# Kernel optimization log

Hardware: AMD Instinct MI355X
Metric: run time of the kernel (lower is better)

Reference implementation:

```python
import jax, jax.numpy as jnp
import numpy as np

T, B, D, H = 2048, 64, 256, 512

def setup_inputs() -> dict:
    key = jax.random.key(0)
    ks = jax.random.split(key, 4)
    s = 1.0 / np.sqrt(D + H)  # nn.Linear default uniform scale approximated with normal*s
    return {
        "x": jax.random.normal(ks[0], (T, B, D), dtype=jnp.float32),
        "h0": jnp.zeros((B, H), dtype=jnp.float32),
        "Wz": jax.random.normal(ks[1], (D + H, H), dtype=jnp.float32) * s,
        "bz": jnp.zeros((H,), dtype=jnp.float32),
        "Wr": jax.random.normal(ks[2], (D + H, H), dtype=jnp.float32) * s,
        "br": jnp.zeros((H,), dtype=jnp.float32),
        "Wh": jax.random.normal(ks[3], (D + H, H), dtype=jnp.float32) * s,
        "bh": jnp.zeros((H,), dtype=jnp.float32),
    }

def reference(x, h0, Wz, bz, Wr, br, Wh, bh):
    """GRU over time: x [T,B,D], h0 [B,H]; returns hidden history [T,B,H]."""
    def step(h, xt):
        xh = jnp.concatenate([xt, h], axis=-1)          # [B, D+H]
        z = jax.nn.sigmoid(xh @ Wz + bz)                # update gate
        r = jax.nn.sigmoid(xh @ Wr + br)                # reset gate
        xrh = jnp.concatenate([xt, r * h], axis=-1)     # [B, D+H]
        h_tilde = jnp.tanh(xrh @ Wh + bh)               # candidate state
        h_new = (1.0 - z) * h + z * h_tilde
        return h_new, h_new
    _, hist = jax.lax.scan(step, h0, x)
    return hist
```

## Files before the change

kernel.cpp:

```cpp
#include <hip/hip_runtime.h>
#include <stdint.h>


#define T_STEPS 2048
#define B_SZ    64
#define D_SZ    256
#define H_SZ    512
#define NGROUP  4
#define NWG     64
#define MB      16
#define CPW     6

typedef __attribute__((ext_vector_type(8))) short  short8;
typedef __attribute__((ext_vector_type(4))) float  f32x4;

__device__ __forceinline__ unsigned short f2bf(float v) {
  uint32_t u = __float_as_uint(v);
  return (unsigned short)((u + 0x7fffu + ((u >> 16) & 1u)) >> 16);
}
__device__ __forceinline__ float bf2f(unsigned short h) {
  return __uint_as_float(((uint32_t)h) << 16);
}
__device__ __forceinline__ void splitf(float v, short& hi, short& lo) {
  unsigned short h = f2bf(v);
  hi = (short)h;
  lo = (short)f2bf(v - bf2f(h));
}
__device__ __forceinline__ uint32_t packf(float v) {
  unsigned short h = f2bf(v);
  unsigned short l = f2bf(v - bf2f(h));
  return ((uint32_t)h << 16) | (uint32_t)l;
}
__device__ __forceinline__ float unpackf(uint32_t p) {
  return __uint_as_float(p & 0xffff0000u) + __uint_as_float(p << 16);
}

__device__ __forceinline__ uint32_t aload32(const uint32_t* p) {
  return __hip_atomic_load(p, __ATOMIC_RELAXED, __HIP_MEMORY_SCOPE_AGENT);
}
__device__ __forceinline__ unsigned long long aload64(const uint32_t* p) {
  return __hip_atomic_load((const unsigned long long*)p, __ATOMIC_RELAXED,
                           __HIP_MEMORY_SCOPE_AGENT);
}
__device__ __forceinline__ void astore32(uint32_t* p, uint32_t v) {
  __hip_atomic_store(p, v, __ATOMIC_RELAXED, __HIP_MEMORY_SCOPE_AGENT);
}

__device__ __forceinline__ void poll_ge(const uint32_t* p, uint32_t tgt, int& cap) {
  int guard = 0;
  for (;;) {
    if (aload32(p) >= tgt) break;
    if (++guard > cap) { cap = 256; break; }
    __builtin_amdgcn_s_sleep(1);
  }
}

__global__ void __launch_bounds__(256, 1)
gru_persistent(const float* __restrict__ x, const float* __restrict__ h0,
               const float* __restrict__ Wz, const float* __restrict__ bz,
               const float* __restrict__ Wr, const float* __restrict__ br,
               const float* __restrict__ Wh, const float* __restrict__ bh,
               float* __restrict__ out,
               uint32_t* zr_ctr, uint32_t* h_ctr,
               uint32_t* h_pk, uint32_t* rh_pk, uint32_t* z_pk)
{
  __shared__ float partT[16 * 64];
  __shared__ float bias1s[16];
  __shared__ float bias2s[8];

  const int tid  = threadIdx.x;
  const int wv   = tid >> 6;
  const int lane = tid & 63;
  const int blk  = blockIdx.x;
  const int g    = blk >> 6;
  const int wid  = blk & 63;
  const int m0   = g * MB;
  const bool isZ = (wid < 32);
  const int c1   = (wid & 31) * 16;
  const int c2   = wid * 8;
  const float* W1 = isZ ? Wz : Wr;

  const int n     = lane & 15;
  const int kq    = lane >> 4;
  const int bfrag = m0 + n;
  const int m2    = kq * 4 + wv;
  const int n2    = n;
  const int b2    = m0 + m2;

  uint32_t* my_zr = zr_ctr + g * 64;
  uint32_t* my_h  = h_ctr  + g * 64;

  short8 w1h[CPW], w1l[CPW], w2h[CPW], w2l[CPW];
  #pragma unroll
  for (int i = 0; i < CPW; ++i) {
    const int ch = wv * CPW + i;
    #pragma unroll
    for (int j = 0; j < 8; ++j) {
      const int k = ch * 32 + kq * 8 + j;
      short hi, lo;
      splitf(W1[(size_t)k * H_SZ + c1 + n], hi, lo);
      w1h[i][j] = hi; w1l[i][j] = lo;
      float v = (n < 8) ? Wh[(size_t)k * H_SZ + c2 + n] : 0.f;
      splitf(v, hi, lo);
      w2h[i][j] = hi; w2l[i][j] = lo;
    }
  }
  if (tid < 16)      bias1s[tid] = isZ ? bz[c1 + tid] : br[c1 + tid];
  else if (tid < 24) bias2s[tid - 16] = bh[c2 + (tid - 16)];
  __syncthreads();

  float hreg = (n2 < 8) ? h0[(size_t)b2 * H_SZ + c2 + n2] : 0.f;

  int cap = 1 << 20;

  #pragma unroll 1
  for (int t = 0; t < T_STEPS; ++t) {
    short8 ah[CPW], al[CPW];

    #pragma unroll
    for (int i = 0; i < CPW; ++i) {
      const int ch = wv * CPW + i;
      if (ch < 8) {
        const float* xp = x + ((size_t)t * B_SZ + bfrag) * D_SZ + ch * 32 + kq * 8;
        float4 f0 = *(const float4*)xp;
        float4 f1 = *(const float4*)(xp + 4);
        float f[8] = {f0.x, f0.y, f0.z, f0.w, f1.x, f1.y, f1.z, f1.w};
        #pragma unroll
        for (int j = 0; j < 8; ++j) { short hi, lo; splitf(f[j], hi, lo); ah[i][j] = hi; al[i][j] = lo; }
      }
    }

    if (t > 0) poll_ge(my_h, (uint32_t)t * NWG, cap);

    uint32_t hpu = 0; float hp0 = 0.f;
    if (!isZ) {
      if (t > 0) hpu = aload32(h_pk + (size_t)b2 * H_SZ + c1 + n2);
      else       hp0 = h0[(size_t)b2 * H_SZ + c1 + n2];
    }

    #pragma unroll
    for (int i = 0; i < CPW; ++i) {
      const int ch = wv * CPW + i;
      if (ch >= 8) {
        const int kh = ch * 32 - 256 + kq * 8;
        if (t > 0) {
          const uint32_t* hp = h_pk + (size_t)bfrag * H_SZ + kh;
          unsigned long long q0 = aload64(hp),     q1 = aload64(hp + 2);
          unsigned long long q2 = aload64(hp + 4), q3 = aload64(hp + 6);
          uint32_t u[8] = {(uint32_t)q0, (uint32_t)(q0 >> 32), (uint32_t)q1, (uint32_t)(q1 >> 32),
                           (uint32_t)q2, (uint32_t)(q2 >> 32), (uint32_t)q3, (uint32_t)(q3 >> 32)};
          #pragma unroll
          for (int j = 0; j < 8; ++j) { ah[i][j] = (short)(u[j] >> 16); al[i][j] = (short)(u[j] & 0xffffu); }
        } else {
          const float* hp = h0 + (size_t)bfrag * H_SZ + kh;
          float4 f0 = *(const float4*)hp;
          float4 f1 = *(const float4*)(hp + 4);
          float f[8] = {f0.x, f0.y, f0.z, f0.w, f1.x, f1.y, f1.z, f1.w};
          #pragma unroll
          for (int j = 0; j < 8; ++j) { short hi, lo; splitf(f[j], hi, lo); ah[i][j] = hi; al[i][j] = lo; }
        }
      }
    }

    {
      f32x4 acc = {0.f, 0.f, 0.f, 0.f};
      #pragma unroll
      for (int i = 0; i < CPW; ++i) {
        acc = __builtin_amdgcn_mfma_f32_16x16x32_bf16(ah[i], w1h[i], acc, 0, 0, 0);
        acc = __builtin_amdgcn_mfma_f32_16x16x32_bf16(al[i], w1h[i], acc, 0, 0, 0);
        acc = __builtin_amdgcn_mfma_f32_16x16x32_bf16(ah[i], w1l[i], acc, 0, 0, 0);
      }
      #pragma unroll
      for (int r = 0; r < 4; ++r) partT[(wv * 4 + r) * 64 + lane] = acc[r];
    }
    __syncthreads();

    {
      float s = partT[(0 + wv) * 64 + lane] + partT[(4 + wv) * 64 + lane]
              + partT[(8 + wv) * 64 + lane] + partT[(12 + wv) * 64 + lane] + bias1s[n2];
      float sg = 1.f / (1.f + __expf(-s));
      if (isZ) {
        astore32(z_pk + (size_t)b2 * H_SZ + c1 + n2, __float_as_uint(sg));
      } else {
        float hp = (t > 0) ? unpackf(hpu) : hp0;
        astore32(rh_pk + (size_t)b2 * H_SZ + c1 + n2, packf(sg * hp));
      }
    }
    asm volatile("s_waitcnt vmcnt(0)" ::: "memory");
    __syncthreads();
    if (tid == 0)
      __hip_atomic_fetch_add(my_zr, 1u, __ATOMIC_RELAXED, __HIP_MEMORY_SCOPE_AGENT);

    poll_ge(my_zr, (uint32_t)(t + 1) * NWG, cap);

    uint32_t zu = 0;
    if (n2 < 8) zu = aload32(z_pk + (size_t)b2 * H_SZ + c2 + n2);

    #pragma unroll
    for (int i = 0; i < CPW; ++i) {
      const int ch = wv * CPW + i;
      if (ch >= 8) {
        const int kh = ch * 32 - 256 + kq * 8;
        const uint32_t* rp = rh_pk + (size_t)bfrag * H_SZ + kh;
        unsigned long long q0 = aload64(rp),     q1 = aload64(rp + 2);
        unsigned long long q2 = aload64(rp + 4), q3 = aload64(rp + 6);
        uint32_t u[8] = {(uint32_t)q0, (uint32_t)(q0 >> 32), (uint32_t)q1, (uint32_t)(q1 >> 32),
                         (uint32_t)q2, (uint32_t)(q2 >> 32), (uint32_t)q3, (uint32_t)(q3 >> 32)};
        #pragma unroll
        for (int j = 0; j < 8; ++j) { ah[i][j] = (short)(u[j] >> 16); al[i][j] = (short)(u[j] & 0xffffu); }
      }
    }

    {
      f32x4 acc = {0.f, 0.f, 0.f, 0.f};
      #pragma unroll
      for (int i = 0; i < CPW; ++i) {
        acc = __builtin_amdgcn_mfma_f32_16x16x32_bf16(ah[i], w2h[i], acc, 0, 0, 0);
        acc = __builtin_amdgcn_mfma_f32_16x16x32_bf16(al[i], w2h[i], acc, 0, 0, 0);
        acc = __builtin_amdgcn_mfma_f32_16x16x32_bf16(ah[i], w2l[i], acc, 0, 0, 0);
      }
      #pragma unroll
      for (int r = 0; r < 4; ++r) partT[(wv * 4 + r) * 64 + lane] = acc[r];
    }
    __syncthreads();

    if (n2 < 8) {
      float s = partT[(0 + wv) * 64 + lane] + partT[(4 + wv) * 64 + lane]
              + partT[(8 + wv) * 64 + lane] + partT[(12 + wv) * 64 + lane] + bias2s[n2];
      float e  = __expf(2.f * s);
      float ht = 1.f - 2.f / (e + 1.f);
      float zf = __uint_as_float(zu);
      float hn = (1.f - zf) * hreg + zf * ht;
      hreg = hn;
      __builtin_nontemporal_store(hn, out + ((size_t)t * B_SZ + b2) * H_SZ + c2 + n2);
      astore32(h_pk + (size_t)b2 * H_SZ + c2 + n2, packf(hn));
    }
    asm volatile("s_waitcnt vmcnt(0)" ::: "memory");
    __syncthreads();
    if (tid == 0)
      __hip_atomic_fetch_add(my_h, 1u, __ATOMIC_RELAXED, __HIP_MEMORY_SCOPE_AGENT);
  }
}

extern "C" void kernel_launch(void* const* d_in, const int* in_sizes, int n_in,
                              void* d_out, int out_size, void* d_ws, size_t ws_size,
                              hipStream_t stream) {
  const float* x  = (const float*)d_in[0];
  const float* h0 = (const float*)d_in[1];
  const float* Wz = (const float*)d_in[2];
  const float* bz = (const float*)d_in[3];
  const float* Wr = (const float*)d_in[4];
  const float* br = (const float*)d_in[5];
  const float* Wh = (const float*)d_in[6];
  const float* bh = (const float*)d_in[7];
  float* out = (float*)d_out;

  char* ws = (char*)d_ws;
  uint32_t* zr_ctr = (uint32_t*)(ws + 0);
  uint32_t* h_ctr  = (uint32_t*)(ws + 16384);
  uint32_t* h_pk   = (uint32_t*)(ws + 32768);
  uint32_t* rh_pk  = (uint32_t*)(ws + 163840);
  uint32_t* z_pk   = (uint32_t*)(ws + 294912);

  hipMemsetAsync(d_ws, 0, 32768, stream);
  gru_persistent<<<dim3(NGROUP * NWG), dim3(256), 0, stream>>>(
      x, h0, Wz, bz, Wr, br, Wh, bh, out,
      zr_ctr, h_ctr, h_pk, rh_pk, z_pk);
}
```

Measured before the change: 27.54 ms.

## Replace atomic counter barrier with per-workgroup flag array polled wavewide

Each workgroup now signals step completion by storing the step number into its own flag slot instead of doing an atomic fetch-add on a shared counter. Waiters poll all 64 flags with one lane per flag and a wave vote, which removes atomic contention on a single address. The output store to global memory is moved after the flag publish so the store-drain wait before signalling covers only the h_pk writes. The cost is more loads per poll iteration, and the relaxed ordering of the late output store needs care.

```diff
diff --git a/kernel.cpp b/kernel.cpp
--- a/kernel.cpp
+++ b/kernel.cpp
@@ -46,10 +46,12 @@
   __hip_atomic_store(p, v, __ATOMIC_RELAXED, __HIP_MEMORY_SCOPE_AGENT);
 }
 
-__device__ __forceinline__ void poll_ge(const uint32_t* p, uint32_t tgt, int& cap) {
+__device__ __forceinline__ void poll_flags(const uint32_t* fl, uint32_t tgt,
+                                           int lane, int& cap) {
   int guard = 0;
   for (;;) {
-    if (aload32(p) >= tgt) break;
+    uint32_t v = aload32(fl + lane);
+    if (__all((int)(v >= tgt))) break;
     if (++guard > cap) { cap = 256; break; }
     __builtin_amdgcn_s_sleep(1);
   }
@@ -61,7 +63,7 @@
                const float* __restrict__ Wr, const float* __restrict__ br,
                const float* __restrict__ Wh, const float* __restrict__ bh,
                float* __restrict__ out,
-               uint32_t* zr_ctr, uint32_t* h_ctr,
+               uint32_t* zr_flg, uint32_t* h_flg,
                uint32_t* h_pk, uint32_t* rh_pk, uint32_t* z_pk)
 {
   __shared__ float partT[16 * 64];
@@ -87,8 +89,8 @@
   const int n2    = n;
   const int b2    = m0 + m2;
 
-  uint32_t* my_zr = zr_ctr + g * 64;
-  uint32_t* my_h  = h_ctr  + g * 64;
+  uint32_t* my_zr = zr_flg + g * 64;
+  uint32_t* my_h  = h_flg  + g * 64;
 
   short8 w1h[CPW], w1l[CPW], w2h[CPW], w2l[CPW];
   #pragma unroll
@@ -130,7 +132,7 @@
       }
     }
 
-    if (t > 0) poll_ge(my_h, (uint32_t)t * NWG, cap);
+    if (t > 0) poll_flags(my_h, (uint32_t)t, lane, cap);
 
     uint32_t hpu = 0; float hp0 = 0.f;
     if (!isZ) {
@@ -188,10 +190,9 @@
     }
     asm volatile("s_waitcnt vmcnt(0)" ::: "memory");
     __syncthreads();
-    if (tid == 0)
-      __hip_atomic_fetch_add(my_zr, 1u, __ATOMIC_RELAXED, __HIP_MEMORY_SCOPE_AGENT);
-
-    poll_ge(my_zr, (uint32_t)(t + 1) * NWG, cap);
+    if (tid == 0) astore32(my_zr + wid, (uint32_t)(t + 1));
+
+    poll_flags(my_zr, (uint32_t)(t + 1), lane, cap);
 
     uint32_t zu = 0;
     if (n2 < 8) zu = aload32(z_pk + (size_t)b2 * H_SZ + c2 + n2);
@@ -224,21 +225,23 @@
     }
     __syncthreads();
 
-    if (n2 < 8) {
+    float hn = 0.f; bool live = (n2 < 8);
+    if (live) {
       float s = partT[(0 + wv) * 64 + lane] + partT[(4 + wv) * 64 + lane]
               + partT[(8 + wv) * 64 + lane] + partT[(12 + wv) * 64 + lane] + bias2s[n2];
       float e  = __expf(2.f * s);
       float ht = 1.f - 2.f / (e + 1.f);
       float zf = __uint_as_float(zu);
-      float hn = (1.f - zf) * hreg + zf * ht;
+      hn = (1.f - zf) * hreg + zf * ht;
       hreg = hn;
+      astore32(h_pk + (size_t)b2 * H_SZ + c2 + n2, packf(hn));
+    }
+    asm volatile("s_waitcnt vmcnt(0)" ::: "memory");
+    __syncthreads();
+    if (tid == 0) astore32(my_h + wid, (uint32_t)(t + 1));
+
+    if (live)
       __builtin_nontemporal_store(hn, out + ((size_t)t * B_SZ + b2) * H_SZ + c2 + n2);
-      astore32(h_pk + (size_t)b2 * H_SZ + c2 + n2, packf(hn));
-    }
-    asm volatile("s_waitcnt vmcnt(0)" ::: "memory");
-    __syncthreads();
-    if (tid == 0)
-      __hip_atomic_fetch_add(my_h, 1u, __ATOMIC_RELAXED, __HIP_MEMORY_SCOPE_AGENT);
   }
 }
 
@@ -256,8 +259,8 @@
   float* out = (float*)d_out;
 
   char* ws = (char*)d_ws;
-  uint32_t* zr_ctr = (uint32_t*)(ws + 0);
-  uint32_t* h_ctr  = (uint32_t*)(ws + 16384);
+  uint32_t* zr_flg = (uint32_t*)(ws + 0);
+  uint32_t* h_flg  = (uint32_t*)(ws + 16384);
   uint32_t* h_pk   = (uint32_t*)(ws + 32768);
   uint32_t* rh_pk  = (uint32_t*)(ws + 163840);
   uint32_t* z_pk   = (uint32_t*)(ws + 294912);
@@ -265,5 +268,5 @@
   hipMemsetAsync(d_ws, 0, 32768, stream);
   gru_persistent<<<dim3(NGROUP * NWG), dim3(256), 0, stream>>>(
       x, h0, Wz, bz, Wr, br, Wh, bh, out,
-      zr_ctr, h_ctr, h_pk, rh_pk, z_pk);
-}
+      zr_flg, h_flg, h_pk, rh_pk, z_pk);
+}
```

New measurement: 25.18 ms. 1.09x faster.
